# Kernel optimization log

Hardware: AMD Instinct MI355X
Metric: run time of the kernel (lower is better)

Reference implementation:

```python
import jax, jax.numpy as jnp
import numpy as np

N, E, H = 6144, 64, 8
D = E * H  # 512
EPS = 1e-5


def _layernorm(v, g, b):
    m = jnp.mean(v, axis=-1, keepdims=True)
    var = jnp.mean((v - m) ** 2, axis=-1, keepdims=True)
    return (v - m) * jax.lax.rsqrt(var + EPS) * g + b


def setup_inputs() -> dict:
    key = jax.random.key(0)
    ks = jax.random.split(key, 4)
    x = jax.random.normal(ks[0], (N, E), dtype=jnp.float32)
    batch = jnp.sort(jax.random.randint(ks[1], (N,), 0, 256)).astype(jnp.int64)
    W_qkv = jax.random.normal(ks[2], (E, 3 * D), dtype=jnp.float32) * (1.0 / np.sqrt(E))
    b_qkv = jnp.zeros((3 * D,), dtype=jnp.float32)
    W_out = jax.random.normal(ks[3], (D, E), dtype=jnp.float32) * (1.0 / np.sqrt(D))
    b_out = jnp.zeros((E,), dtype=jnp.float32)
    return {
        "x": x, "batch": batch,
        "ln1_g": jnp.ones((E,), jnp.float32), "ln1_b": jnp.zeros((E,), jnp.float32),
        "W_qkv": W_qkv, "b_qkv": b_qkv,
        "ln2_g": jnp.ones((D,), jnp.float32), "ln2_b": jnp.zeros((D,), jnp.float32),
        "W_out": W_out, "b_out": b_out,
    }


def reference(x, batch, ln1_g, ln1_b, W_qkv, b_qkv, ln2_g, ln2_b, W_out, b_out):
    n = x.shape[0]
    h1 = _layernorm(x, ln1_g, ln1_b)                       # [N, E]
    kqv = h1 @ W_qkv + b_qkv                               # [N, 3D]
    K, Q, V = jnp.split(kqv, 3, axis=-1)                   # each [N, D], order K,Q,V per torch split
    # 'n (h d) -> h n d' with per-head dim d = E
    Q = Q.reshape(n, H, E).transpose(1, 0, 2)
    K = K.reshape(n, H, E).transpose(1, 0, 2)
    V = V.reshape(n, H, E).transpose(1, 0, 2)
    scores = jnp.einsum('hnd,hmd->hnm', Q, K) / np.sqrt(D)  # NOTE: scale by sqrt(D)=sqrt(H*E), as in source
    mask = batch[None, :, None] == batch[None, None, :]     # block-diagonal per-graph mask
    scores = jnp.where(mask, scores, -jnp.inf)
    attn = jax.nn.softmax(scores, axis=-1)                  # [H, N, N]
    out = jnp.einsum('hnm,hmd->hnd', attn, V)               # [H, N, E]
    out = out.transpose(1, 0, 2).reshape(n, D)              # 'h n d -> n (h d)'
    y = _layernorm(out, ln2_g, ln2_b) @ W_out + b_out       # out_proj with use_norm_layer=True
    return y
```

## Files before the change

kernel.cpp:

```cpp
#include <hip/hip_runtime.h>
#include <math.h>

#define N 6144
#define E 64
#define H 8
#define D 512
#define TD 1536
#define EPS 1e-5f
#define SCALE 0.04419417382415922f
#define RMAX 80

typedef __attribute__((ext_vector_type(8))) short bf16x8;
typedef __attribute__((ext_vector_type(4))) float f32x4;

static __device__ __forceinline__ unsigned short f2bf(float f) {
    union { float f; unsigned int u; } v; v.f = f;
    unsigned int r = v.u + 0x7FFFu + ((v.u >> 16) & 1u);
    return (unsigned short)(r >> 16);
}
static __device__ __forceinline__ float bf2f(unsigned short u) {
    union { unsigned int u; float f; } v; v.u = ((unsigned int)u) << 16;
    return v.f;
}

__global__ __launch_bounds__(256) void prep_kernel(
    const float* __restrict__ x, const float* __restrict__ ln1g,
    const float* __restrict__ ln1b, const float* __restrict__ W_qkv,
    const float* __restrict__ W_out, const int* __restrict__ batch,
    unsigned short* __restrict__ Wt, unsigned short* __restrict__ Wot,
    int* __restrict__ bound, unsigned short* __restrict__ h1g)
{
    const int t = threadIdx.x, lane = t & 63, wv = t >> 6;
    if (blockIdx.x < 32) {
        const int tid = blockIdx.x * 256 + t;
        if (tid < N) {
            const int bv = batch[tid];
            const int prev = tid ? batch[tid - 1] : -1;
            if (bv != prev)
                for (int v = prev + 1; v <= bv; ++v) bound[v] = tid;
            if (tid == N - 1)
                for (int v = bv + 1; v <= 256; ++v) bound[v] = N;
        }
        for (int i = tid; i < 64 * TD; i += 8192) {
            const int k = i / TD, j = i - k * TD;
            Wt[j * 64 + k] = f2bf(W_qkv[i]);
        }
        for (int i = tid; i < 512 * 64; i += 8192) {
            const int k = i >> 6, j = i & 63;
            Wot[j * 512 + k] = f2bf(W_out[i]);
        }
    } else {
        const int row = (blockIdx.x - 32) * 4 + wv;
        const float v = x[(size_t)row * E + lane];
        float sm = v, sq = v * v;
        #pragma unroll
        for (int off = 1; off < 64; off <<= 1) {
            sm += __shfl_xor(sm, off);
            sq += __shfl_xor(sq, off);
        }
        const float mean = sm * (1.f / 64.f);
        const float var  = sq * (1.f / 64.f) - mean * mean;
        h1g[(size_t)row * 64 + lane] =
            f2bf((v - mean) * rsqrtf(var + EPS) * ln1g[lane] + ln1b[lane]);
    }
}

__global__ __launch_bounds__(256) void seghead_kernel(
    const unsigned short* __restrict__ h1g, const unsigned short* __restrict__ Wt,
    const float* __restrict__ b_qkv, const int* __restrict__ bound,
    unsigned short* __restrict__ attb)
{
    __shared__ unsigned short Qs[RMAX][72];
    __shared__ unsigned short Ks[RMAX][72];
    __shared__ unsigned short Vs[64][104];
    __shared__ unsigned short Ps[RMAX][104];

    const int t = threadIdx.x, lane = t & 63, wv = t >> 6;
    const int lr = lane & 15, lg = lane >> 4;
    const int b = blockIdx.x, h = blockIdx.y;

    const int ct = wv;
    const int jK = h * 64 + ct * 16;
    const int jQ = 512 + jK;
    const int jV = 1024 + jK;
    const bf16x8 wK0 = *(const bf16x8*)&Wt[(size_t)(jK + lr) * 64 + lg * 8];
    const bf16x8 wK1 = *(const bf16x8*)&Wt[(size_t)(jK + lr) * 64 + 32 + lg * 8];
    const bf16x8 wQ0 = *(const bf16x8*)&Wt[(size_t)(jQ + lr) * 64 + lg * 8];
    const bf16x8 wQ1 = *(const bf16x8*)&Wt[(size_t)(jQ + lr) * 64 + 32 + lg * 8];
    const bf16x8 wV0 = *(const bf16x8*)&Wt[(size_t)(jV + lr) * 64 + lg * 8];
    const bf16x8 wV1 = *(const bf16x8*)&Wt[(size_t)(jV + lr) * 64 + 32 + lg * 8];
    const float bK = b_qkv[jK + lr];
    const float bQ = b_qkv[jQ + lr];
    const float bV = b_qkv[jV + lr];

    const int s = bound[b];
    int R = bound[b + 1] - s;
    if (R <= 0) return;
    if (R > RMAX) R = RMAX;
    const int NT = (R + 15) >> 4;
    const int RT = NT * 16;
    const int KB = (RT + 31) >> 5;

    if (RT < KB * 32) {
        for (int idx = t; idx < 64 * 16; idx += 256) {
            const int dd = idx >> 4, cc = RT + (idx & 15);
            if (cc < KB * 32) Vs[dd][cc] = 0;
        }
    }

    #pragma unroll
    for (int rt = 0; rt < 5; ++rt) {
        if (rt < NT) {
            int row = s + rt * 16 + lr;
            row = row < N ? row : N - 1;
            const bf16x8 a0 = *(const bf16x8*)&h1g[(size_t)row * 64 + lg * 8];
            const bf16x8 a1 = *(const bf16x8*)&h1g[(size_t)row * 64 + 32 + lg * 8];
            f32x4 dK = {0,0,0,0}, dQ = {0,0,0,0}, dV = {0,0,0,0};
            dK = __builtin_amdgcn_mfma_f32_16x16x32_bf16(a0, wK0, dK, 0, 0, 0);
            dK = __builtin_amdgcn_mfma_f32_16x16x32_bf16(a1, wK1, dK, 0, 0, 0);
            dQ = __builtin_amdgcn_mfma_f32_16x16x32_bf16(a0, wQ0, dQ, 0, 0, 0);
            dQ = __builtin_amdgcn_mfma_f32_16x16x32_bf16(a1, wQ1, dQ, 0, 0, 0);
            dV = __builtin_amdgcn_mfma_f32_16x16x32_bf16(a0, wV0, dV, 0, 0, 0);
            dV = __builtin_amdgcn_mfma_f32_16x16x32_bf16(a1, wV1, dV, 0, 0, 0);
            const int n4 = rt * 16 + lg * 4;
            #pragma unroll
            for (int r = 0; r < 4; ++r) {
                Ks[n4 + r][ct * 16 + lr] = f2bf(dK[r] + bK);
                Qs[n4 + r][ct * 16 + lr] = f2bf(dQ[r] + bQ);
            }
            union { unsigned short us[4]; uint2 u2; } pk;
            #pragma unroll
            for (int r = 0; r < 4; ++r) pk.us[r] = f2bf(dV[r] + bV);
            *(uint2*)&Vs[ct * 16 + lr][n4] = pk.u2;
        }
    }
    __syncthreads();

    bf16x8 ones;
    #pragma unroll
    for (int j = 0; j < 8; ++j) ones[j] = (short)0x3F80;

    for (int qt = wv; qt < NT; qt += 4) {
        const bf16x8 qf0 = *(const bf16x8*)&Qs[qt * 16 + lr][lg * 8];
        const bf16x8 qf1 = *(const bf16x8*)&Qs[qt * 16 + lr][32 + lg * 8];
        for (int kt = 0; kt < 2 * KB; ++kt) {
            if (kt < NT) {
                const bf16x8 kf0 = *(const bf16x8*)&Ks[kt * 16 + lr][lg * 8];
                const bf16x8 kf1 = *(const bf16x8*)&Ks[kt * 16 + lr][32 + lg * 8];
                f32x4 dsc = {0.f, 0.f, 0.f, 0.f};
                dsc = __builtin_amdgcn_mfma_f32_16x16x32_bf16(qf0, kf0, dsc, 0, 0, 0);
                dsc = __builtin_amdgcn_mfma_f32_16x16x32_bf16(qf1, kf1, dsc, 0, 0, 0);
                const bool valid = (kt * 16 + lr) < R;
                #pragma unroll
                for (int r = 0; r < 4; ++r)
                    Ps[qt * 16 + lg * 4 + r][kt * 16 + lr] =
                        valid ? f2bf(__expf(dsc[r] * SCALE)) : 0;
            } else {
                #pragma unroll
                for (int r = 0; r < 4; ++r)
                    Ps[qt * 16 + lg * 4 + r][kt * 16 + lr] = 0;
            }
        }
        asm volatile("s_waitcnt lgkmcnt(0)" ::: "memory");

        f32x4 o0 = {0,0,0,0}, o1 = {0,0,0,0}, o2 = {0,0,0,0}, o3 = {0,0,0,0};
        f32x4 sac = {0,0,0,0};
        for (int kb = 0; kb < KB; ++kb) {
            const bf16x8 pa = *(const bf16x8*)&Ps[qt * 16 + lr][kb * 32 + lg * 8];
            sac = __builtin_amdgcn_mfma_f32_16x16x32_bf16(pa, ones, sac, 0, 0, 0);
            const bf16x8 v0 = *(const bf16x8*)&Vs[lr][kb * 32 + lg * 8];
            const bf16x8 v1 = *(const bf16x8*)&Vs[16 + lr][kb * 32 + lg * 8];
            const bf16x8 v2 = *(const bf16x8*)&Vs[32 + lr][kb * 32 + lg * 8];
            const bf16x8 v3 = *(const bf16x8*)&Vs[48 + lr][kb * 32 + lg * 8];
            o0 = __builtin_amdgcn_mfma_f32_16x16x32_bf16(pa, v0, o0, 0, 0, 0);
            o1 = __builtin_amdgcn_mfma_f32_16x16x32_bf16(pa, v1, o1, 0, 0, 0);
            o2 = __builtin_amdgcn_mfma_f32_16x16x32_bf16(pa, v2, o2, 0, 0, 0);
            o3 = __builtin_amdgcn_mfma_f32_16x16x32_bf16(pa, v3, o3, 0, 0, 0);
        }

        #pragma unroll
        for (int r = 0; r < 4; ++r) {
            const float inv = 1.f / sac[r];
            const int q = qt * 16 + lg * 4 + r;
            Ps[q][lr]      = f2bf(o0[r] * inv);
            Ps[q][16 + lr] = f2bf(o1[r] * inv);
            Ps[q][32 + lr] = f2bf(o2[r] * inv);
            Ps[q][48 + lr] = f2bf(o3[r] * inv);
        }
        asm volatile("s_waitcnt lgkmcnt(0)" ::: "memory");
        #pragma unroll
        for (int pass = 0; pass < 2; ++pass) {
            const int qi = pass * 8 + (lane >> 3);
            const int q  = qt * 16 + qi;
            const int dd = (lane & 7) * 8;
            if (q < R)
                *(bf16x8*)(attb + (size_t)(s + q) * D + h * 64 + dd) =
                    *(const bf16x8*)&Ps[q][dd];
        }
    }
}

__global__ __launch_bounds__(256) void ln2_out_kernel(
    const unsigned short* __restrict__ att, const float* __restrict__ g,
    const float* __restrict__ b, const unsigned short* __restrict__ Wot,
    const float* __restrict__ bias, float* __restrict__ y)
{
    __shared__ unsigned short h2[16][520];
    const int t = threadIdx.x, lane = t & 63, wv = t >> 6;
    const int row0 = blockIdx.x * 16;
    const int lr = lane & 15, lg = lane >> 4;

    const float4 ga = *(const float4*)&g[lane * 8];
    const float4 gb = *(const float4*)&g[lane * 8 + 4];
    const float4 ba = *(const float4*)&b[lane * 8];
    const float4 bb = *(const float4*)&b[lane * 8 + 4];
    const float gv[8] = {ga.x, ga.y, ga.z, ga.w, gb.x, gb.y, gb.z, gb.w};
    const float bv[8] = {ba.x, ba.y, ba.z, ba.w, bb.x, bb.y, bb.z, bb.w};

    #pragma unroll
    for (int i = 0; i < 4; ++i) {
        const int r = wv * 4 + i;
        const bf16x8 v8 = *(const bf16x8*)(att + (size_t)(row0 + r) * D + lane * 8);
        float vals[8];
        float sm = 0.f, sq = 0.f;
        #pragma unroll
        for (int c = 0; c < 8; ++c) {
            vals[c] = bf2f((unsigned short)v8[c]);
            sm += vals[c];
            sq += vals[c] * vals[c];
        }
        #pragma unroll
        for (int off = 1; off < 64; off <<= 1) {
            sm += __shfl_xor(sm, off);
            sq += __shfl_xor(sq, off);
        }
        const float mean = sm * (1.f / 512.f);
        const float var  = sq * (1.f / 512.f) - mean * mean;
        const float rstd = rsqrtf(var + EPS);
        bf16x8 hv;
        #pragma unroll
        for (int c = 0; c < 8; ++c)
            hv[c] = (short)f2bf((vals[c] - mean) * rstd * gv[c] + bv[c]);
        *(bf16x8*)&h2[r][lane * 8] = hv;
    }
    __syncthreads();

    const int j0 = wv * 16;
    f32x4 acc = {0.f, 0.f, 0.f, 0.f};
    #pragma unroll
    for (int ks = 0; ks < 16; ++ks) {
        const bf16x8 a  = *(const bf16x8*)&h2[lr][ks * 32 + lg * 8];
        const bf16x8 wb = *(const bf16x8*)&Wot[(size_t)(j0 + lr) * D + ks * 32 + lg * 8];
        acc = __builtin_amdgcn_mfma_f32_16x16x32_bf16(a, wb, acc, 0, 0, 0);
    }
    const float bj = bias[j0 + lr];
    #pragma unroll
    for (int r = 0; r < 4; ++r)
        y[(size_t)(row0 + lg * 4 + r) * 64 + j0 + lr] = acc[r] + bj;
}

extern "C" void kernel_launch(void* const* d_in, const int* in_sizes, int n_in,
                              void* d_out, int out_size, void* d_ws, size_t ws_size,
                              hipStream_t stream) {
    const float* x     = (const float*)d_in[0];
    const int*   batch = (const int*)  d_in[1];
    const float* ln1_g = (const float*)d_in[2];
    const float* ln1_b = (const float*)d_in[3];
    const float* W_qkv = (const float*)d_in[4];
    const float* b_qkv = (const float*)d_in[5];
    const float* ln2_g = (const float*)d_in[6];
    const float* ln2_b = (const float*)d_in[7];
    const float* W_out = (const float*)d_in[8];
    const float* b_out = (const float*)d_in[9];
    float* y = (float*)d_out;

    unsigned short* Wt   = (unsigned short*)d_ws;
    unsigned short* Wot  = Wt  + (size_t)TD * 64;
    unsigned short* h1g  = Wot + (size_t)64 * D;
    unsigned short* attb = h1g + (size_t)N * 64;
    int* bound = (int*)(attb + (size_t)N * D);

    hipLaunchKernelGGL(prep_kernel, dim3(1568), dim3(256), 0, stream,
                       x, ln1_g, ln1_b, W_qkv, W_out, batch, Wt, Wot, bound, h1g);
    hipLaunchKernelGGL(seghead_kernel, dim3(256, 8), dim3(256), 0, stream,
                       h1g, Wt, b_qkv, bound, attb);
    hipLaunchKernelGGL(ln2_out_kernel, dim3(N / 16), dim3(256), 0, stream,
                       attb, ln2_g, ln2_b, Wot, b_out, y);
}
```

Measured before the change: 35.32 us.

## Fuse LayerNorm1 into the per-segment attention kernel, staging normalized rows in LDS

The first LayerNorm moves out of the prep kernel and into the segment-head kernel, which normalizes its own rows from x straight into shared memory by reusing the Ps buffer. This removes the h1g global round trip and shrinks the prep kernel to 32 blocks. In exchange, each of the 8 head blocks per segment recomputes the same LayerNorm, and an extra __syncthreads is added. Launch bounds now also request 3 blocks per SM.

```diff
diff --git a/kernel.cpp b/kernel.cpp
--- a/kernel.cpp
+++ b/kernel.cpp
@@ -24,49 +24,32 @@
 }
 
 __global__ __launch_bounds__(256) void prep_kernel(
+    const float* __restrict__ W_qkv, const float* __restrict__ W_out,
+    const int* __restrict__ batch, unsigned short* __restrict__ Wt,
+    unsigned short* __restrict__ Wot, int* __restrict__ bound)
+{
+    const int tid = blockIdx.x * 256 + threadIdx.x;
+    if (tid < N) {
+        const int bv = batch[tid];
+        const int prev = tid ? batch[tid - 1] : -1;
+        if (bv != prev)
+            for (int v = prev + 1; v <= bv; ++v) bound[v] = tid;
+        if (tid == N - 1)
+            for (int v = bv + 1; v <= 256; ++v) bound[v] = N;
+    }
+    for (int i = tid; i < 64 * TD; i += 8192) {
+        const int k = i / TD, j = i - k * TD;
+        Wt[j * 64 + k] = f2bf(W_qkv[i]);
+    }
+    for (int i = tid; i < 512 * 64; i += 8192) {
+        const int k = i >> 6, j = i & 63;
+        Wot[j * 512 + k] = f2bf(W_out[i]);
+    }
+}
+
+__global__ __launch_bounds__(256, 3) void seghead_kernel(
     const float* __restrict__ x, const float* __restrict__ ln1g,
-    const float* __restrict__ ln1b, const float* __restrict__ W_qkv,
-    const float* __restrict__ W_out, const int* __restrict__ batch,
-    unsigned short* __restrict__ Wt, unsigned short* __restrict__ Wot,
-    int* __restrict__ bound, unsigned short* __restrict__ h1g)
-{
-    const int t = threadIdx.x, lane = t & 63, wv = t >> 6;
-    if (blockIdx.x < 32) {
-        const int tid = blockIdx.x * 256 + t;
-        if (tid < N) {
-            const int bv = batch[tid];
-            const int prev = tid ? batch[tid - 1] : -1;
-            if (bv != prev)
-                for (int v = prev + 1; v <= bv; ++v) bound[v] = tid;
-            if (tid == N - 1)
-                for (int v = bv + 1; v <= 256; ++v) bound[v] = N;
-        }
-        for (int i = tid; i < 64 * TD; i += 8192) {
-            const int k = i / TD, j = i - k * TD;
-            Wt[j * 64 + k] = f2bf(W_qkv[i]);
-        }
-        for (int i = tid; i < 512 * 64; i += 8192) {
-            const int k = i >> 6, j = i & 63;
-            Wot[j * 512 + k] = f2bf(W_out[i]);
-        }
-    } else {
-        const int row = (blockIdx.x - 32) * 4 + wv;
-        const float v = x[(size_t)row * E + lane];
-        float sm = v, sq = v * v;
-        #pragma unroll
-        for (int off = 1; off < 64; off <<= 1) {
-            sm += __shfl_xor(sm, off);
-            sq += __shfl_xor(sq, off);
-        }
-        const float mean = sm * (1.f / 64.f);
-        const float var  = sq * (1.f / 64.f) - mean * mean;
-        h1g[(size_t)row * 64 + lane] =
-            f2bf((v - mean) * rsqrtf(var + EPS) * ln1g[lane] + ln1b[lane]);
-    }
-}
-
-__global__ __launch_bounds__(256) void seghead_kernel(
-    const unsigned short* __restrict__ h1g, const unsigned short* __restrict__ Wt,
+    const float* __restrict__ ln1b, const unsigned short* __restrict__ Wt,
     const float* __restrict__ b_qkv, const int* __restrict__ bound,
     unsigned short* __restrict__ attb)
 {
@@ -74,6 +57,7 @@
     __shared__ unsigned short Ks[RMAX][72];
     __shared__ unsigned short Vs[64][104];
     __shared__ unsigned short Ps[RMAX][104];
+    unsigned short (*h1s)[72] = (unsigned short(*)[72])Ps;
 
     const int t = threadIdx.x, lane = t & 63, wv = t >> 6;
     const int lr = lane & 15, lg = lane >> 4;
@@ -101,20 +85,35 @@
     const int RT = NT * 16;
     const int KB = (RT + 31) >> 5;
 
+    {
+        const float gv = ln1g[lane], bv = ln1b[lane];
+        for (int i = wv; i < RT; i += 4) {
+            int row = s + i; row = row < N ? row : N - 1;
+            const float v = x[(size_t)row * E + lane];
+            float sm = v, sq = v * v;
+            #pragma unroll
+            for (int off = 1; off < 64; off <<= 1) {
+                sm += __shfl_xor(sm, off);
+                sq += __shfl_xor(sq, off);
+            }
+            const float mean = sm * (1.f / 64.f);
+            const float var  = sq * (1.f / 64.f) - mean * mean;
+            h1s[i][lane] = f2bf((v - mean) * rsqrtf(var + EPS) * gv + bv);
+        }
+    }
     if (RT < KB * 32) {
         for (int idx = t; idx < 64 * 16; idx += 256) {
             const int dd = idx >> 4, cc = RT + (idx & 15);
             if (cc < KB * 32) Vs[dd][cc] = 0;
         }
     }
+    __syncthreads();
 
     #pragma unroll
     for (int rt = 0; rt < 5; ++rt) {
         if (rt < NT) {
-            int row = s + rt * 16 + lr;
-            row = row < N ? row : N - 1;
-            const bf16x8 a0 = *(const bf16x8*)&h1g[(size_t)row * 64 + lg * 8];
-            const bf16x8 a1 = *(const bf16x8*)&h1g[(size_t)row * 64 + 32 + lg * 8];
+            const bf16x8 a0 = *(const bf16x8*)&h1s[rt * 16 + lr][lg * 8];
+            const bf16x8 a1 = *(const bf16x8*)&h1s[rt * 16 + lr][32 + lg * 8];
             f32x4 dK = {0,0,0,0}, dQ = {0,0,0,0}, dV = {0,0,0,0};
             dK = __builtin_amdgcn_mfma_f32_16x16x32_bf16(a0, wK0, dK, 0, 0, 0);
             dK = __builtin_amdgcn_mfma_f32_16x16x32_bf16(a1, wK1, dK, 0, 0, 0);
@@ -276,14 +275,13 @@
 
     unsigned short* Wt   = (unsigned short*)d_ws;
     unsigned short* Wot  = Wt  + (size_t)TD * 64;
-    unsigned short* h1g  = Wot + (size_t)64 * D;
-    unsigned short* attb = h1g + (size_t)N * 64;
+    unsigned short* attb = Wot + (size_t)64 * D;
     int* bound = (int*)(attb + (size_t)N * D);
 
-    hipLaunchKernelGGL(prep_kernel, dim3(1568), dim3(256), 0, stream,
-                       x, ln1_g, ln1_b, W_qkv, W_out, batch, Wt, Wot, bound, h1g);
+    hipLaunchKernelGGL(prep_kernel, dim3(32), dim3(256), 0, stream,
+                       W_qkv, W_out, batch, Wt, Wot, bound);
     hipLaunchKernelGGL(seghead_kernel, dim3(256, 8), dim3(256), 0, stream,
-                       h1g, Wt, b_qkv, bound, attb);
+                       x, ln1_g, ln1_b, Wt, b_qkv, bound, attb);
     hipLaunchKernelGGL(ln2_out_kernel, dim3(N / 16), dim3(256), 0, stream,
                        attb, ln2_g, ln2_b, Wot, b_out, y);
 }
```

After: 44.04 us. 24.7% more time.
